# Kernel tuning notes

Measured on AMD Instinct MI355X. Metric: run time of the kernel, lower is better.

The kernel has to match this reference:

```python
import jax, jax.numpy as jnp
import numpy as np

N = 8192
BACKBONE_DIM = 384
PCD_FEAT_DIM = 6
OUT_DIM = 384
WIDTH = 384
N_HID_INST = 6
N_HID_POS = 4
MARGIN = 1.0
MAX_GROUPING_SCALE = 2.0
EPS_NORM = 1e-5
EPS_D2 = 1e-12


def setup_inputs() -> dict:
    key = jax.random.key(0)
    ks = jax.random.split(key, 12)
    s = 0.05  # ~1/sqrt(384) fan-in init
    inp = {
        "point_selected_feat": jax.random.normal(ks[0], (N, BACKBONE_DIM), jnp.float32),
        "point_orgfeat": jax.random.normal(ks[1], (N, PCD_FEAT_DIM), jnp.float32),
        "scale": jax.random.uniform(ks[2], (N, 1), jnp.float32, 0.0, 2.0),
        "mask_id": jax.random.randint(ks[3], (N,), 0, 64, jnp.int64 if jax.config.jax_enable_x64 else jnp.int32),
        "rand_u": jax.random.uniform(ks[4], (1,), jnp.float32),
        "chunk_size": 256,
        "inst_W_in": jax.random.normal(ks[5], (BACKBONE_DIM + 1, WIDTH), jnp.float32) * s,
        "inst_W_hid": jax.random.normal(ks[6], (N_HID_INST - 1, WIDTH, WIDTH), jnp.float32) * s,
        "inst_W_out": jax.random.normal(ks[7], (WIDTH, OUT_DIM), jnp.float32) * s,
        "pos_W_in": jax.random.normal(ks[8], (PCD_FEAT_DIM + 1, WIDTH), jnp.float32) * s,
        "pos_W_hid": jax.random.normal(ks[9], (N_HID_POS - 1, WIDTH, WIDTH), jnp.float32) * s,
        "pos_W_out": jax.random.normal(ks[10], (WIDTH, OUT_DIM), jnp.float32) * s,
    }
    return inp


def _mlp(x, W_in, W_hid, W_out):
    h = jax.nn.relu(x @ W_in)
    def body(h, W):
        return jax.nn.relu(h @ W), None
    h, _ = jax.lax.scan(body, h, W_hid)
    return h @ W_out


def _normed(x):
    n = jnp.linalg.norm(x, axis=-1, keepdims=True)
    return x / (n + EPS_NORM)


def _embed(feat_sel, feat_org, s, iWi, iWh, iWo, pWi, pWh, pWo):
    # quantile_transformer is fit externally at runtime; identity here
    inst = _normed(_mlp(jnp.concatenate([feat_sel, s], axis=-1), iWi, iWh, iWo))
    pos = _normed(_mlp(jnp.concatenate([feat_org, s], axis=-1), pWi, pWh, pWo))
    return inst + pos


def _chunk_pdist(emb, C, S):
    # pairwise L2 distances within each chunk via gram trick: [C,S,S]
    z = emb.reshape(C, S, -1)
    sq = jnp.sum(z * z, axis=-1)                      # [C,S]
    g = jnp.einsum("csd,ctd->cst", z, z)              # [C,S,S]
    d2 = sq[:, :, None] + sq[:, None, :] - 2.0 * g
    return jnp.sqrt(jnp.where(d2 > EPS_D2, d2, EPS_D2))


def _masked_mean(vals, mask):
    cnt = jnp.maximum(jnp.sum(mask), 1).astype(vals.dtype)
    return jnp.sum(vals * mask) / cnt


def reference(point_selected_feat, point_orgfeat, scale, mask_id, rand_u, chunk_size,
              inst_W_in, inst_W_hid, inst_W_out, pos_W_in, pos_W_hid, pos_W_out):
    S = chunk_size
    C = point_selected_feat.shape[0] // S

    lab = mask_id.reshape(C, S)
    eq = lab[:, :, None] == lab[:, None, :]                       # label equality within chunk
    valid = lab != -1
    valid_pair = valid[:, :, None] & valid[:, None, :]
    triu = jnp.triu(jnp.ones((S, S), dtype=bool), k=0)            # block_mask after triu(diag=0)
    block = triu[None] & valid_pair                               # [C,S,S]
    diag = jnp.eye(S, dtype=bool)[None]
    pos_mask = (eq & block & ~diag).astype(jnp.float32)
    neg_mask = ((~eq) & block).astype(jnp.float32)
    sum_block = jnp.sum(block).astype(jnp.float32)

    w_pos = jnp.sum(pos_mask) / sum_block
    w_neg = jnp.sum(neg_mask) / sum_block

    args = (inst_W_in, inst_W_hid, inst_W_out, pos_W_in, pos_W_hid, pos_W_out)

    # loss 1 (and loss 3 reuses the same embedding: original recomputes identically)
    emb = _embed(point_selected_feat, point_orgfeat, scale, *args)
    dist = _chunk_pdist(emb, C, S)
    loss1 = _masked_mean(dist, pos_mask)
    loss3 = _masked_mean(jax.nn.relu(MARGIN - dist), neg_mask)

    # hierarchy loss at a randomly enlarged scale
    scale_diff = jnp.maximum(0.0, MAX_GROUPING_SCALE - scale)
    larger_scale = scale + scale_diff * rand_u
    emb2 = _embed(point_selected_feat, point_orgfeat, larger_scale, *args)
    dist2 = _chunk_pdist(emb2, C, S)
    loss2 = _masked_mean(dist2, pos_mask)

    total = loss1 * w_pos + loss2 * w_pos + loss3 * w_neg
    return total
```

## Files before the change

### kernel.cpp

```cpp
#include <hip/hip_runtime.h>
#include <math.h>

#define NPTS 8192
#define DIMW 384
#define MB   64
#define LDH  448
#define KIN  416
#define KPOS 32
#define SCH  256
#define NCH  32
#define LZB  136
#define EWAVES 12
#define ETHREADS (EWAVES * 64)

typedef __attribute__((ext_vector_type(8))) short bf16x8;
typedef __attribute__((ext_vector_type(4))) float f32x4;
typedef __attribute__((ext_vector_type(4))) unsigned short us4;
typedef __attribute__((ext_vector_type(8))) unsigned short us8;

#define WLOAD(dst, ptr) \
  asm volatile("global_load_dwordx4 %0, %1, off" : "=v"(dst) : "v"(ptr) : "memory")
#define WWAIT() do { \
  asm volatile("s_waitcnt vmcnt(0)" ::: "memory"); \
  __builtin_amdgcn_sched_barrier(0); } while (0)

#define SZ_HID   (384*384)
#define OFF_IIN  0
#define SZ_IIN   (384*416)
#define OFF_IHID (OFF_IIN + SZ_IIN)
#define OFF_IOUT (OFF_IHID + 5*SZ_HID)
#define OFF_PIN  (OFF_IOUT + SZ_HID)
#define SZ_PIN   (384*32)
#define OFF_PHID (OFF_PIN + SZ_PIN)
#define OFF_POUT (OFF_PHID + 3*SZ_HID)
#define WTS_USHORTS (OFF_POUT + SZ_HID)
#define WTS_BYTES   ((size_t)WTS_USHORTS * 2)
#define EMB_US      ((size_t)NPTS * DIMW)
#define EMB_BYTES   (EMB_US * 2)

__device__ __forceinline__ ushort f2bf(float x) {
  union { float f; unsigned u; } v; v.f = x;
  unsigned r = v.u + 0x7FFF + ((v.u >> 16) & 1);
  return (ushort)(r >> 16);
}
__device__ __forceinline__ float bf2f(ushort u) {
  union { unsigned u; float f; } v; v.u = ((unsigned)u) << 16; return v.f;
}

__global__ __launch_bounds__(256) void convert_wts_swz(
    const float* __restrict__ iWin, const float* __restrict__ iWhid,
    const float* __restrict__ iWout, const float* __restrict__ pWin,
    const float* __restrict__ pWhid, const float* __restrict__ pWout,
    ushort* __restrict__ wts) {
  const int seg = blockIdx.y;
  const float* src; ushort* dst; int Ksrc, NKl;
  if (seg == 0)      { src = iWin;  dst = wts + OFF_IIN;  Ksrc = 385; NKl = 13; }
  else if (seg <= 5) { src = iWhid + (size_t)(seg-1)*SZ_HID; dst = wts + OFF_IHID + (size_t)(seg-1)*SZ_HID; Ksrc = 384; NKl = 12; }
  else if (seg == 6) { src = iWout; dst = wts + OFF_IOUT; Ksrc = 384; NKl = 12; }
  else if (seg == 7) { src = pWin;  dst = wts + OFF_PIN;  Ksrc = 7;   NKl = 1;  }
  else if (seg <= 10){ src = pWhid + (size_t)(seg-8)*SZ_HID; dst = wts + OFF_PHID + (size_t)(seg-8)*SZ_HID; Ksrc = 384; NKl = 12; }
  else               { src = pWout; dst = wts + OFF_POUT; Ksrc = 384; NKl = 12; }
  const int t = blockIdx.x * 256 + threadIdx.x;
  if (t >= NKl * 1536) return;
  const int lane = t & 63;
  const int frag = t >> 6;
  const int i = frag & 1;
  const int rest = frag >> 1;
  const int ks = rest % NKl;
  const int wave = rest / NKl;
  const int n  = wave * 32 + i * 16 + (lane & 15);
  const int kb = ks * 32 + (lane >> 4) * 8;
  us8 o;
#pragma unroll
  for (int e = 0; e < 8; ++e) {
    const int k = kb + e;
    o[e] = (k < Ksrc) ? f2bf(src[(size_t)k * 384 + n]) : (ushort)0;
  }
  *(us8*)&dst[(size_t)t * 8] = o;
}

template <int NK, bool STORE>
__device__ __forceinline__ void mlayer(const ushort* __restrict__ Wt,
    const ushort* __restrict__ bin, ushort* __restrict__ bout,
    int wave, int lane, int lr, int lq, int n0, f32x4 acc[2][4]) {
#pragma unroll
  for (int i = 0; i < 2; ++i)
#pragma unroll
    for (int j = 0; j < 4; ++j) acc[i][j] = (f32x4)(0.f);

  constexpr int NC = (NK + 3) / 4;
  bf16x8 w[2][4][2], h[2][4];
  const ushort* wp = Wt + (size_t)wave * NK * 1024 + lane * 8;
  const int swz = lr & 7;
  const ushort* hbase = bin + lr * LDH;

#pragma unroll
  for (int s = 0; s < 4; ++s)
    if (s < NK) {
      WLOAD(w[0][s][0], wp + s * 1024);
      WLOAD(w[0][s][1], wp + s * 1024 + 512);
    }
#pragma unroll
  for (int j = 0; j < 4; ++j)
    h[0][j] = *(const bf16x8*)(hbase + j * 16 * LDH + ((lq ^ swz) << 3));
  WWAIT();

#pragma unroll
  for (int c = 0; c < NC; ++c) {
    if (c + 1 < NC) {
#pragma unroll
      for (int s = 0; s < 4; ++s)
        if ((c + 1) * 4 + s < NK) {
          WLOAD(w[(c + 1) & 1][s][0], wp + (size_t)((c + 1) * 4 + s) * 1024);
          WLOAD(w[(c + 1) & 1][s][1], wp + (size_t)((c + 1) * 4 + s) * 1024 + 512);
        }
      __builtin_amdgcn_sched_barrier(0);
    }
#pragma unroll
    for (int s = 0; s < 4; ++s) {
      const int ks = c * 4 + s;
      if (ks < NK) {
        if (ks + 1 < NK) {
#pragma unroll
          for (int j = 0; j < 4; ++j)
            h[(ks + 1) & 1][j] = *(const bf16x8*)(hbase + j * 16 * LDH + ((((ks + 1) * 4 + lq) ^ swz) << 3));
        }
#pragma unroll
        for (int j = 0; j < 4; ++j)
#pragma unroll
          for (int i = 0; i < 2; ++i)
            acc[i][j] = __builtin_amdgcn_mfma_f32_16x16x32_bf16(w[c & 1][s][i], h[ks & 1][j], acc[i][j], 0, 0, 0);
      }
    }
    if (c + 1 < NC) WWAIT();
  }
  if (STORE) {
#pragma unroll
    for (int i = 0; i < 2; ++i)
#pragma unroll
      for (int j = 0; j < 4; ++j) {
        f32x4 a = acc[i][j];
        us4 o;
        o[0] = f2bf(fmaxf(a[0], 0.f));
        o[1] = f2bf(fmaxf(a[1], 0.f));
        o[2] = f2bf(fmaxf(a[2], 0.f));
        o[3] = f2bf(fmaxf(a[3], 0.f));
        const int col = n0 + i * 16 + lq * 4;
        const int slot = col >> 3;
        *(us4*)&bout[(j * 16 + lr) * LDH + (((slot ^ swz) << 3) | ((lq & 1) << 2))] = o;
      }
    __syncthreads();
  }
}

__device__ __forceinline__ void norm_store(f32x4 acc[2][4], ushort* __restrict__ embp,
    bool add, int lr, int lq, int wave, int n0, float (*wsum)[64], float* invn) {
#pragma unroll
  for (int j = 0; j < 4; ++j) {
    float s = 0.f;
#pragma unroll
    for (int i = 0; i < 2; ++i) {
      f32x4 a = acc[i][j];
      s = fmaf(a[0], a[0], s); s = fmaf(a[1], a[1], s);
      s = fmaf(a[2], a[2], s); s = fmaf(a[3], a[3], s);
    }
    s += __shfl_xor(s, 16, 64);
    s += __shfl_xor(s, 32, 64);
    if (lq == 0) wsum[wave][j * 16 + lr] = s;
  }
  __syncthreads();
  if (threadIdx.x < 64) {
    float tot = 0.f;
#pragma unroll
    for (int w = 0; w < EWAVES; ++w) tot += wsum[w][threadIdx.x];
    invn[threadIdx.x] = 1.f / (sqrtf(tot) + 1e-5f);
  }
  __syncthreads();
#pragma unroll
  for (int j = 0; j < 4; ++j) {
    const float inv = invn[j * 16 + lr];
#pragma unroll
    for (int i = 0; i < 2; ++i) {
      ushort* p = embp + (size_t)(j * 16 + lr) * DIMW + n0 + i * 16 + lq * 4;
      float o0 = acc[i][j][0] * inv, o1 = acc[i][j][1] * inv;
      float o2 = acc[i][j][2] * inv, o3 = acc[i][j][3] * inv;
      if (add) {
        us4 old = *(const us4*)p;
        o0 += bf2f(old[0]); o1 += bf2f(old[1]);
        o2 += bf2f(old[2]); o3 += bf2f(old[3]);
      }
      us4 o; o[0] = f2bf(o0); o[1] = f2bf(o1); o[2] = f2bf(o2); o[3] = f2bf(o3);
      *(us4*)p = o;
    }
  }
  __syncthreads();
}

__global__ __launch_bounds__(ETHREADS, 3) void embed_mfma(
    const float* __restrict__ feat_sel, const float* __restrict__ feat_org,
    const float* __restrict__ scale, const float* __restrict__ rand_u,
    const ushort* __restrict__ wts, ushort* __restrict__ emb) {
  __shared__ ushort bufA[MB * LDH];
  __shared__ ushort bufB[MB * LDH];
  __shared__ float s_lds[MB];
  __shared__ float wsum[EWAVES][64];
  __shared__ float invn[64];

  const int t = threadIdx.x;
  const int p0 = blockIdx.x * MB;
  const int var = blockIdx.y;
  ushort* embp = emb + (size_t)var * EMB_US + (size_t)p0 * DIMW;

  if (t < MB) {
    float s = scale[p0 + t];
    if (var) s += fmaxf(0.f, 2.f - s) * rand_u[0];
    s_lds[t] = s;
  }
#pragma unroll
  for (int it = 0; it < 8; ++it) {
    int idx = t + it * ETHREADS;
    int m = idx / 96, kq = idx - m * 96;
    const float4 v = *(const float4*)&feat_sel[(size_t)(p0 + m) * DIMW + kq * 4];
    us4 o; o[0] = f2bf(v.x); o[1] = f2bf(v.y); o[2] = f2bf(v.z); o[3] = f2bf(v.w);
    const int ph = (((kq >> 1) ^ (m & 7)) << 3) | ((kq & 1) << 2);
    *(us4*)&bufA[m * LDH + ph] = o;
  }
  if (t < MB) {
    us8 z = (us8)(0);
#pragma unroll
    for (int q = 48; q < 56; ++q) *(us8*)&bufA[t * LDH + q * 8] = z;
    bufA[t * LDH + 384 + (t & 7) * 8] = f2bf(s_lds[t]);
  }
  __syncthreads();

  const int lane = t & 63, wave = t >> 6;
  const int lr = lane & 15, lq = lane >> 4;
  const int n0 = wave * 32;
  f32x4 acc[2][4];

  mlayer<13, true >(wts + OFF_IIN,             bufA, bufB, wave, lane, lr, lq, n0, acc);
  mlayer<12, true >(wts + OFF_IHID + 0*SZ_HID, bufB, bufA, wave, lane, lr, lq, n0, acc);
  mlayer<12, true >(wts + OFF_IHID + 1*SZ_HID, bufA, bufB, wave, lane, lr, lq, n0, acc);
  mlayer<12, true >(wts + OFF_IHID + 2*SZ_HID, bufB, bufA, wave, lane, lr, lq, n0, acc);
  mlayer<12, true >(wts + OFF_IHID + 3*SZ_HID, bufA, bufB, wave, lane, lr, lq, n0, acc);
  mlayer<12, true >(wts + OFF_IHID + 4*SZ_HID, bufB, bufA, wave, lane, lr, lq, n0, acc);
  mlayer<12, false>(wts + OFF_IOUT,            bufA, bufB, wave, lane, lr, lq, n0, acc);
  norm_store(acc, embp, false, lr, lq, wave, n0, wsum, invn);

  if (t < MB) {
    const float* fo = feat_org + (size_t)(p0 + t) * 6;
    us8 b0;
#pragma unroll
    for (int k = 0; k < 6; ++k) b0[k] = f2bf(fo[k]);
    b0[6] = f2bf(s_lds[t]);
    b0[7] = 0;
    us8 z = (us8)(0);
    const int e = t & 7;
    *(us8*)&bufA[t * LDH + ((0 ^ e) << 3)] = b0;
    *(us8*)&bufA[t * LDH + ((1 ^ e) << 3)] = z;
    *(us8*)&bufA[t * LDH + ((2 ^ e) << 3)] = z;
    *(us8*)&bufA[t * LDH + ((3 ^ e) << 3)] = z;
  }
  __syncthreads();

  mlayer<1,  true >(wts + OFF_PIN,             bufA, bufB, wave, lane, lr, lq, n0, acc);
  mlayer<12, true >(wts + OFF_PHID + 0*SZ_HID, bufB, bufA, wave, lane, lr, lq, n0, acc);
  mlayer<12, true >(wts + OFF_PHID + 1*SZ_HID, bufA, bufB, wave, lane, lr, lq, n0, acc);
  mlayer<12, true >(wts + OFF_PHID + 2*SZ_HID, bufB, bufA, wave, lane, lr, lq, n0, acc);
  mlayer<12, false>(wts + OFF_POUT,            bufA, bufB, wave, lane, lr, lq, n0, acc);
  norm_store(acc, embp, true, lr, lq, wave, n0, wsum, invn);
}

__global__ __launch_bounds__(512) void dist_mfma(
    const ushort* __restrict__ emb, const int* __restrict__ mask_id,
    float* __restrict__ part) {
  __shared__ ushort zb[SCH * LZB];
  __shared__ float sqv[SCH];
  __shared__ int labv[SCH];
  __shared__ float scratch[8];

  const int c = blockIdx.x, hh = blockIdx.y, v = blockIdx.z;
  const int t = threadIdx.x;
  const ushort* embc = emb + (size_t)v * EMB_US + (size_t)c * SCH * DIMW;

  if (t < SCH) labv[t] = mask_id[c * SCH + t];

  const int lane = t & 63, wave = t >> 6;
  const int lr = lane & 15, lq = lane >> 4;
  const int wa = wave >> 2, wb = wave & 3;

  f32x4 acc[4][4];
#pragma unroll
  for (int i = 0; i < 4; ++i)
#pragma unroll
    for (int j = 0; j < 4; ++j) acc[i][j] = (f32x4)(0.f);

  const int sr = t >> 1, sh = (t & 1) * 64;
  float sq = 0.f;

  for (int kc = 0; kc < 3; ++kc) {
    __syncthreads();
    const ushort* zrow = embc + (size_t)sr * DIMW + kc * 128 + sh;
    ushort* zd = zb + sr * LZB + sh;
#pragma unroll
    for (int q = 0; q < 8; ++q) {
      us8 x = *(const us8*)&zrow[q * 8];
      *(us8*)&zd[q * 8] = x;
#pragma unroll
      for (int e = 0; e < 8; ++e) { float f = bf2f(x[e]); sq = fmaf(f, f, sq); }
    }
    __syncthreads();
    const ushort* ap = zb + (hh * 128 + wa * 64 + lr) * LZB + lq * 8;
    const ushort* bp = zb + (wb * 64 + lr) * LZB + lq * 8;
#pragma unroll
    for (int ks = 0; ks < 4; ++ks) {
      bf16x8 af[4], bfr[4];
#pragma unroll
      for (int i = 0; i < 4; ++i) af[i] = *(const bf16x8*)(ap + i * 16 * LZB + ks * 32);
#pragma unroll
      for (int j = 0; j < 4; ++j) bfr[j] = *(const bf16x8*)(bp + j * 16 * LZB + ks * 32);
#pragma unroll
      for (int j = 0; j < 4; ++j)
#pragma unroll
        for (int i = 0; i < 4; ++i)
          acc[i][j] = __builtin_amdgcn_mfma_f32_16x16x32_bf16(af[i], bfr[j], acc[i][j], 0, 0, 0);
    }
  }
  sq += __shfl_xor(sq, 1, 64);
  if (!(t & 1)) sqv[sr] = sq;
  __syncthreads();

  float s_pos = 0.f, s_neg = 0.f, c_pos = 0.f, c_neg = 0.f, c_blk = 0.f;
#pragma unroll
  for (int i = 0; i < 4; ++i) {
    const int ib = hh * 128 + wa * 64 + i * 16 + lq * 4;
#pragma unroll
    for (int j = 0; j < 4; ++j) {
      const int jG = wb * 64 + j * 16 + lr;
      const int lj = labv[jG];
      const float sqj = sqv[jG];
#pragma unroll
      for (int vv = 0; vv < 4; ++vv) {
        const int iG = ib + vv;
        const int li = labv[iG];
        if (li != -1 && lj != -1 && iG <= jG) {
          c_blk += 1.f;
          if (iG < jG) {
            float d2 = sqv[iG] + sqj - 2.f * acc[i][j][vv];
            float d = sqrtf(fmaxf(d2, 1e-12f));
            if (li == lj) { s_pos += d; c_pos += 1.f; }
            else          { s_neg += fmaxf(1.f - d, 0.f); c_neg += 1.f; }
          }
        }
      }
    }
  }
  float vals[5] = { s_pos, s_neg, c_pos, c_neg, c_blk };
  float res[5];
#pragma unroll
  for (int r = 0; r < 5; ++r) {
    float x = vals[r];
#pragma unroll
    for (int o = 32; o > 0; o >>= 1) x += __shfl_xor(x, o, 64);
    __syncthreads();
    if ((t & 63) == 0) scratch[t >> 6] = x;
    __syncthreads();
    float s = 0.f;
#pragma unroll
    for (int w = 0; w < 8; ++w) s += scratch[w];
    res[r] = s;
  }
  if (t == 0) {
    float* pb = part + (size_t)((v * 2 + hh) * NCH + c) * 8;
    pb[0] = res[0]; pb[1] = res[1]; pb[2] = res[2]; pb[3] = res[3]; pb[4] = res[4];
  }
}

__global__ __launch_bounds__(128) void final_kernel(
    const float* __restrict__ part, float* __restrict__ out) {
  __shared__ float scratch[2];
  const int t = threadIdx.x;
  const float* pb = part + (size_t)t * 8;
  const bool v0 = t < 64;
  float sp1 = v0 ? pb[0] : 0.f;
  float sp2 = v0 ? 0.f : pb[0];
  float sn  = v0 ? pb[1] : 0.f;
  float cp  = v0 ? pb[2] : 0.f;
  float cn  = v0 ? pb[3] : 0.f;
  float cb  = v0 ? pb[4] : 0.f;
  float vals[6] = { sp1, sp2, sn, cp, cn, cb };
  float res[6];
#pragma unroll
  for (int r = 0; r < 6; ++r) {
    float x = vals[r];
#pragma unroll
    for (int o = 32; o > 0; o >>= 1) x += __shfl_xor(x, o, 64);
    __syncthreads();
    if ((t & 63) == 0) scratch[t >> 6] = x;
    __syncthreads();
    res[r] = scratch[0] + scratch[1];
  }
  if (t == 0) {
    float l1 = res[0] / fmaxf(res[3], 1.f);
    float l2 = res[1] / fmaxf(res[3], 1.f);
    float l3 = res[2] / fmaxf(res[4], 1.f);
    out[0] = (l1 + l2) * (res[3] / res[5]) + l3 * (res[4] / res[5]);
  }
}

extern "C" void kernel_launch(void* const* d_in, const int* in_sizes, int n_in,
                              void* d_out, int out_size, void* d_ws, size_t ws_size,
                              hipStream_t stream) {
  const float* feat_sel = (const float*)d_in[0];
  const float* feat_org = (const float*)d_in[1];
  const float* scale    = (const float*)d_in[2];
  const int*   mask_id  = (const int*)d_in[3];
  const float* rand_u   = (const float*)d_in[4];
  const float* iWin  = (const float*)d_in[6];
  const float* iWhid = (const float*)d_in[7];
  const float* iWout = (const float*)d_in[8];
  const float* pWin  = (const float*)d_in[9];
  const float* pWhid = (const float*)d_in[10];
  const float* pWout = (const float*)d_in[11];

  ushort* wts = (ushort*)d_ws;
  ushort* emb = (ushort*)((char*)d_ws + WTS_BYTES);
  float*  part = (float*)((char*)d_ws + WTS_BYTES + 2 * EMB_BYTES);

  dim3 gC(78, 12);
  convert_wts_swz<<<gC, 256, 0, stream>>>(iWin, iWhid, iWout, pWin, pWhid, pWout, wts);

  dim3 gE(NPTS / MB, 2);
  embed_mfma<<<gE, ETHREADS, 0, stream>>>(feat_sel, feat_org, scale, rand_u, wts, emb);

  dim3 gD(NCH, 2, 2);
  dist_mfma<<<gD, 512, 0, stream>>>(emb, mask_id, part);

  final_kernel<<<1, 128, 0, stream>>>(part, (float*)d_out);
}
```

Measured before the change: 103.4 us.

## Use 8 waves with 48-column tiles and fine-grained vmcnt waits in MLP kernel

Reworks the embedding MLP kernel so each of 8 waves computes 48 output columns (three 16-wide MFMA fragments) instead of 12 waves computing 32, with matching weight swizzle in the conversion kernel. The weight prefetch now buffers two k-steps and uses graded s_waitcnt vmcnt counts in place of a full drain, so MFMAs can start while later weight loads are still in flight. The aim is more reuse of each LDS activation fragment per wave and less stalling on global weight loads. In exchange it raises register pressure (occupancy hint drops from 3 to 2 blocks) and leaves fewer waves per block to hide latency.

Result: slower. 123.1 us (+19.1%).

```diff
diff --git a/kernel.cpp b/kernel.cpp
--- a/kernel.cpp
+++ b/kernel.cpp
@@ -5,12 +5,10 @@
 #define DIMW 384
 #define MB   64
 #define LDH  448
-#define KIN  416
-#define KPOS 32
 #define SCH  256
 #define NCH  32
 #define LZB  136
-#define EWAVES 12
+#define EWAVES 8
 #define ETHREADS (EWAVES * 64)
 
 typedef __attribute__((ext_vector_type(8))) short bf16x8;
@@ -20,8 +18,8 @@
 
 #define WLOAD(dst, ptr) \
   asm volatile("global_load_dwordx4 %0, %1, off" : "=v"(dst) : "v"(ptr) : "memory")
-#define WWAIT() do { \
-  asm volatile("s_waitcnt vmcnt(0)" ::: "memory"); \
+#define VMW(N) do { \
+  asm volatile("s_waitcnt vmcnt(" #N ")" ::: "memory"); \
   __builtin_amdgcn_sched_barrier(0); } while (0)
 
 #define SZ_HID   (384*384)
@@ -64,11 +62,11 @@
   if (t >= NKl * 1536) return;
   const int lane = t & 63;
   const int frag = t >> 6;
-  const int i = frag & 1;
-  const int rest = frag >> 1;
+  const int i = frag % 3;
+  const int rest = frag / 3;
   const int ks = rest % NKl;
   const int wave = rest / NKl;
-  const int n  = wave * 32 + i * 16 + (lane & 15);
+  const int n  = wave * 48 + i * 16 + (lane & 15);
   const int kb = ks * 32 + (lane >> 4) * 8;
   us8 o;
 #pragma unroll
@@ -82,61 +80,70 @@
 template <int NK, bool STORE>
 __device__ __forceinline__ void mlayer(const ushort* __restrict__ Wt,
     const ushort* __restrict__ bin, ushort* __restrict__ bout,
-    int wave, int lane, int lr, int lq, int n0, f32x4 acc[2][4]) {
-#pragma unroll
-  for (int i = 0; i < 2; ++i)
+    int wave, int lane, int lr, int lq, int n0, f32x4 acc[3][4]) {
+#pragma unroll
+  for (int i = 0; i < 3; ++i)
 #pragma unroll
     for (int j = 0; j < 4; ++j) acc[i][j] = (f32x4)(0.f);
 
-  constexpr int NC = (NK + 3) / 4;
-  bf16x8 w[2][4][2], h[2][4];
-  const ushort* wp = Wt + (size_t)wave * NK * 1024 + lane * 8;
+  constexpr int NC = (NK + 1) / 2;
+  bf16x8 w[2][2][3], h[2][4];
+  const ushort* wp = Wt + (size_t)wave * NK * 1536 + lane * 8;
   const int swz = lr & 7;
   const ushort* hbase = bin + lr * LDH;
 
 #pragma unroll
-  for (int s = 0; s < 4; ++s)
+  for (int s = 0; s < 2; ++s)
     if (s < NK) {
-      WLOAD(w[0][s][0], wp + s * 1024);
-      WLOAD(w[0][s][1], wp + s * 1024 + 512);
+#pragma unroll
+      for (int i = 0; i < 3; ++i)
+        WLOAD(w[0][s][i], wp + (size_t)s * 1536 + i * 512);
     }
 #pragma unroll
   for (int j = 0; j < 4; ++j)
     h[0][j] = *(const bf16x8*)(hbase + j * 16 * LDH + ((lq ^ swz) << 3));
-  WWAIT();
 
 #pragma unroll
   for (int c = 0; c < NC; ++c) {
     if (c + 1 < NC) {
 #pragma unroll
-      for (int s = 0; s < 4; ++s)
-        if ((c + 1) * 4 + s < NK) {
-          WLOAD(w[(c + 1) & 1][s][0], wp + (size_t)((c + 1) * 4 + s) * 1024);
-          WLOAD(w[(c + 1) & 1][s][1], wp + (size_t)((c + 1) * 4 + s) * 1024 + 512);
+      for (int s = 0; s < 2; ++s)
+        if ((c + 1) * 2 + s < NK) {
+#pragma unroll
+          for (int i = 0; i < 3; ++i)
+            WLOAD(w[(c + 1) & 1][s][i], wp + (size_t)((c + 1) * 2 + s) * 1536 + i * 512);
         }
       __builtin_amdgcn_sched_barrier(0);
     }
-#pragma unroll
-    for (int s = 0; s < 4; ++s) {
-      const int ks = c * 4 + s;
+    const int rem_c = NK - 2 * c;
+    const int curI = 3 * (rem_c >= 2 ? 2 : rem_c);
+    const int rem_n = NK - 2 * (c + 1);
+    const int nxtI = (c + 1 < NC) ? 3 * (rem_n >= 2 ? 2 : rem_n) : 0;
+#pragma unroll
+    for (int s = 0; s < 2; ++s) {
+      const int ks = c * 2 + s;
       if (ks < NK) {
         if (ks + 1 < NK) {
 #pragma unroll
           for (int j = 0; j < 4; ++j)
             h[(ks + 1) & 1][j] = *(const bf16x8*)(hbase + j * 16 * LDH + ((((ks + 1) * 4 + lq) ^ swz) << 3));
         }
+        const int N = curI - 3 * (s + 1) + nxtI;
+        if (N >= 9) VMW(9);
+        else if (N >= 6) VMW(6);
+        else if (N >= 3) VMW(3);
+        else             VMW(0);
 #pragma unroll
         for (int j = 0; j < 4; ++j)
 #pragma unroll
-          for (int i = 0; i < 2; ++i)
+          for (int i = 0; i < 3; ++i)
             acc[i][j] = __builtin_amdgcn_mfma_f32_16x16x32_bf16(w[c & 1][s][i], h[ks & 1][j], acc[i][j], 0, 0, 0);
       }
     }
-    if (c + 1 < NC) WWAIT();
   }
   if (STORE) {
 #pragma unroll
-    for (int i = 0; i < 2; ++i)
+    for (int i = 0; i < 3; ++i)
 #pragma unroll
       for (int j = 0; j < 4; ++j) {
         f32x4 a = acc[i][j];
@@ -153,13 +160,13 @@
   }
 }
 
-__device__ __forceinline__ void norm_store(f32x4 acc[2][4], ushort* __restrict__ embp,
+__device__ __forceinline__ void norm_store(f32x4 acc[3][4], ushort* __restrict__ embp,
     bool add, int lr, int lq, int wave, int n0, float (*wsum)[64], float* invn) {
 #pragma unroll
   for (int j = 0; j < 4; ++j) {
     float s = 0.f;
 #pragma unroll
-    for (int i = 0; i < 2; ++i) {
+    for (int i = 0; i < 3; ++i) {
       f32x4 a = acc[i][j];
       s = fmaf(a[0], a[0], s); s = fmaf(a[1], a[1], s);
       s = fmaf(a[2], a[2], s); s = fmaf(a[3], a[3], s);
@@ -180,7 +187,7 @@
   for (int j = 0; j < 4; ++j) {
     const float inv = invn[j * 16 + lr];
 #pragma unroll
-    for (int i = 0; i < 2; ++i) {
+    for (int i = 0; i < 3; ++i) {
       ushort* p = embp + (size_t)(j * 16 + lr) * DIMW + n0 + i * 16 + lq * 4;
       float o0 = acc[i][j][0] * inv, o1 = acc[i][j][1] * inv;
       float o2 = acc[i][j][2] * inv, o3 = acc[i][j][3] * inv;
@@ -196,7 +203,7 @@
   __syncthreads();
 }
 
-__global__ __launch_bounds__(ETHREADS, 3) void embed_mfma(
+__global__ __launch_bounds__(ETHREADS, 2) void embed_mfma(
     const float* __restrict__ feat_sel, const float* __restrict__ feat_org,
     const float* __restrict__ scale, const float* __restrict__ rand_u,
     const ushort* __restrict__ wts, ushort* __restrict__ emb) {
@@ -217,7 +224,7 @@
     s_lds[t] = s;
   }
 #pragma unroll
-  for (int it = 0; it < 8; ++it) {
+  for (int it = 0; it < 12; ++it) {
     int idx = t + it * ETHREADS;
     int m = idx / 96, kq = idx - m * 96;
     const float4 v = *(const float4*)&feat_sel[(size_t)(p0 + m) * DIMW + kq * 4];
@@ -235,8 +242,8 @@
 
   const int lane = t & 63, wave = t >> 6;
   const int lr = lane & 15, lq = lane >> 4;
-  const int n0 = wave * 32;
-  f32x4 acc[2][4];
+  const int n0 = wave * 48;
+  f32x4 acc[3][4];
 
   mlayer<13, true >(wts + OFF_IIN,             bufA, bufB, wave, lane, lr, lq, n0, acc);
   mlayer<12, true >(wts + OFF_IHID + 0*SZ_HID, bufB, bufA, wave, lane, lr, lq, n0, acc);
```

## Rotate per-wave K-chunk order and deepen weight prefetch pipelining in MLP layer

Applied to the files above, without the earlier changes.

Restructures the per-layer GEMM loop so each wave starts its K traversal at a different phase (wave % NC), working in chunks of two K-steps instead of four. This spreads LDS and global accesses across waves. It also swaps the full vmcnt(0) wait for a partial vmcnt(4) wait, so the next chunk's weight loads stay in flight while MFMAs run, and it raises wave priority around the MFMA block. The trade-off is that the runtime-variable chunk index may cost extra address arithmetic, and the loop is harder to unroll statically.

Result: no change. 103.7 us (+0.3%).

```diff
diff --git a/kernel.cpp b/kernel.cpp
--- a/kernel.cpp
+++ b/kernel.cpp
@@ -5,8 +5,6 @@
 #define DIMW 384
 #define MB   64
 #define LDH  448
-#define KIN  416
-#define KPOS 32
 #define SCH  256
 #define NCH  32
 #define LZB  136
@@ -20,8 +18,10 @@
 
 #define WLOAD(dst, ptr) \
   asm volatile("global_load_dwordx4 %0, %1, off" : "=v"(dst) : "v"(ptr) : "memory")
-#define WWAIT() do { \
-  asm volatile("s_waitcnt vmcnt(0)" ::: "memory"); \
+#define WLOAD_O(dst, ptr) \
+  asm volatile("global_load_dwordx4 %0, %1, off offset:1024" : "=v"(dst) : "v"(ptr) : "memory")
+#define VMW(N) do { \
+  asm volatile("s_waitcnt vmcnt(" #N ")" ::: "memory"); \
   __builtin_amdgcn_sched_barrier(0); } while (0)
 
 #define SZ_HID   (384*384)
@@ -88,51 +88,62 @@
 #pragma unroll
     for (int j = 0; j < 4; ++j) acc[i][j] = (f32x4)(0.f);
 
-  constexpr int NC = (NK + 3) / 4;
-  bf16x8 w[2][4][2], h[2][4];
+  constexpr int NC = (NK + 1) / 2;
+  bf16x8 w[2][2][2], h0[4], h1[4];
   const ushort* wp = Wt + (size_t)wave * NK * 1024 + lane * 8;
   const int swz = lr & 7;
   const ushort* hbase = bin + lr * LDH;
-
-#pragma unroll
-  for (int s = 0; s < 4; ++s)
-    if (s < NK) {
-      WLOAD(w[0][s][0], wp + s * 1024);
-      WLOAD(w[0][s][1], wp + s * 1024 + 512);
-    }
-#pragma unroll
-  for (int j = 0; j < 4; ++j)
-    h[0][j] = *(const bf16x8*)(hbase + j * 16 * LDH + ((lq ^ swz) << 3));
-  WWAIT();
-
-#pragma unroll
-  for (int c = 0; c < NC; ++c) {
-    if (c + 1 < NC) {
-#pragma unroll
-      for (int s = 0; s < 4; ++s)
-        if ((c + 1) * 4 + s < NK) {
-          WLOAD(w[(c + 1) & 1][s][0], wp + (size_t)((c + 1) * 4 + s) * 1024);
-          WLOAD(w[(c + 1) & 1][s][1], wp + (size_t)((c + 1) * 4 + s) * 1024 + 512);
-        }
+  const int phase = (NC > 1) ? (wave % NC) : 0;
+
+  {
+    const int ksa = 2 * phase;
+    const int ksb = (2 * phase + 1 < NK) ? 2 * phase + 1 : NK - 1;
+    const ushort* pa = wp + (size_t)ksa * 1024;
+    const ushort* pb = wp + (size_t)ksb * 1024;
+    WLOAD(w[0][0][0], pa); WLOAD_O(w[0][0][1], pa);
+    WLOAD(w[0][1][0], pb); WLOAD_O(w[0][1][1], pb);
+  }
+  int c = phase;
+#pragma unroll
+  for (int i = 0; i < NC; ++i) {
+    const int cn = (c + 1 == NC) ? 0 : c + 1;
+    if (i + 1 < NC) {
+      const int ksa = 2 * cn;
+      const int ksb = (2 * cn + 1 < NK) ? 2 * cn + 1 : NK - 1;
+      const ushort* pa = wp + (size_t)ksa * 1024;
+      const ushort* pb = wp + (size_t)ksb * 1024;
+      WLOAD(w[(i + 1) & 1][0][0], pa); WLOAD_O(w[(i + 1) & 1][0][1], pa);
+      WLOAD(w[(i + 1) & 1][1][0], pb); WLOAD_O(w[(i + 1) & 1][1][1], pb);
       __builtin_amdgcn_sched_barrier(0);
     }
-#pragma unroll
-    for (int s = 0; s < 4; ++s) {
-      const int ks = c * 4 + s;
-      if (ks < NK) {
-        if (ks + 1 < NK) {
-#pragma unroll
-          for (int j = 0; j < 4; ++j)
-            h[(ks + 1) & 1][j] = *(const bf16x8*)(hbase + j * 16 * LDH + ((((ks + 1) * 4 + lq) ^ swz) << 3));
-        }
-#pragma unroll
-        for (int j = 0; j < 4; ++j)
-#pragma unroll
-          for (int i = 0; i < 2; ++i)
-            acc[i][j] = __builtin_amdgcn_mfma_f32_16x16x32_bf16(w[c & 1][s][i], h[ks & 1][j], acc[i][j], 0, 0, 0);
-      }
-    }
-    if (c + 1 < NC) WWAIT();
+    const int ks0 = 2 * c, ks1 = 2 * c + 1;
+    const int ho0 = ((ks0 * 4 + lq) ^ swz) << 3;
+#pragma unroll
+    for (int j = 0; j < 4; ++j)
+      h0[j] = *(const bf16x8*)(hbase + j * 16 * LDH + ho0);
+    const bool do1 = (NK % 2 == 0) || (ks1 < NK);
+    if (do1) {
+      const int ho1 = ((ks1 * 4 + lq) ^ swz) << 3;
+#pragma unroll
+      for (int j = 0; j < 4; ++j)
+        h1[j] = *(const bf16x8*)(hbase + j * 16 * LDH + ho1);
+    }
+    if (i + 1 < NC) VMW(4); else VMW(0);
+    __builtin_amdgcn_s_setprio(1);
+#pragma unroll
+    for (int j = 0; j < 4; ++j)
+#pragma unroll
+      for (int ii = 0; ii < 2; ++ii)
+        acc[ii][j] = __builtin_amdgcn_mfma_f32_16x16x32_bf16(w[i & 1][0][ii], h0[j], acc[ii][j], 0, 0, 0);
+    if (do1) {
+#pragma unroll
+      for (int j = 0; j < 4; ++j)
+#pragma unroll
+        for (int ii = 0; ii < 2; ++ii)
+          acc[ii][j] = __builtin_amdgcn_mfma_f32_16x16x32_bf16(w[i & 1][1][ii], h1[j], acc[ii][j], 0, 0, 0);
+    }
+    __builtin_amdgcn_s_setprio(0);
+    c = cn;
   }
   if (STORE) {
 #pragma unroll
```
